# Optimization experiments

Measured on AMD Instinct MI355X. Metric: run time of the kernel, lower is better.

Reference implementation:

```python
import jax, jax.numpy as jnp
import numpy as np

NEG_SLOPE = 0.2  # PyG GATConv default LeakyReLU slope


def _leaky_relu(x):
    return jnp.where(x >= 0, x, NEG_SLOPE * x)


def gat_conv(x, edge_index, W, a_src, a_dst, b, concat):
    """Faithful PyG GATConv: gather -> leakyrelu attention -> per-dst softmax -> scatter.
    x: [N, Fin], edge_index: [2, E] (src, dst), W: [Fin, H*C], a_src/a_dst: [H, C], b: [H*C] or [C].
    """
    N = x.shape[0]
    H, C = a_src.shape
    src, dst = edge_index[0], edge_index[1]
    h = (x @ W).reshape(N, H, C)                       # [N, H, C]
    alpha_s = jnp.einsum('nhc,hc->nh', h, a_src)       # [N, H]
    alpha_d = jnp.einsum('nhc,hc->nh', h, a_dst)       # [N, H]
    e = _leaky_relu(alpha_s[src] + alpha_d[dst])       # [E, H]
    # numerically stable softmax over edges grouped by destination node
    m = jax.ops.segment_max(e, dst, num_segments=N)    # [N, H]
    e = jnp.exp(e - m[dst])                            # [E, H]
    denom = jax.ops.segment_sum(e, dst, num_segments=N)  # [N, H]
    alpha = e / denom[dst]                             # [E, H]
    msg = h[src] * alpha[:, :, None]                   # [E, H, C]
    out = jax.ops.segment_sum(msg, dst, num_segments=N)  # [N, H, C]
    out = out.reshape(N, H * C) if concat else out.mean(axis=1)
    return out + b


def setup_inputs() -> dict:
    key = jax.random.key(0)
    ks = jax.random.split(key, 12)
    N, E, Fin, Fout = 100000, 1600000, 256, 40
    H1, C1 = 8, 8
    x = jax.random.normal(ks[0], (N, Fin), dtype=jnp.float32)
    edge_index = jax.random.randint(ks[1], (2, E), 0, N, dtype=jnp.int64)
    g = lambda k, shape: jax.random.normal(k, shape, dtype=jnp.float32) * np.float32(np.sqrt(2.0 / (shape[0] + shape[-1])))
    return {
        'x': x,
        'edge_index': edge_index,
        'W1': g(ks[2], (Fin, H1 * C1)),
        'a1_src': g(ks[3], (H1, C1)),
        'a1_dst': g(ks[4], (H1, C1)),
        'b1': jnp.zeros((H1 * C1,), dtype=jnp.float32),
        'W2': g(ks[5], (H1 * C1, Fout)),
        'a2_src': g(ks[6], (1, Fout)),
        'a2_dst': g(ks[7], (1, Fout)),
        'b2': jnp.zeros((Fout,), dtype=jnp.float32),
    }


def reference(x, edge_index, W1, a1_src, a1_dst, b1, W2, a2_src, a2_dst, b2):
    N = x.shape[0]
    # PyG GATConv adds self-loops by default
    loops = jnp.arange(N, dtype=edge_index.dtype)
    ei = jnp.concatenate([edge_index, jnp.stack([loops, loops])], axis=1)
    h = gat_conv(x, ei, W1, a1_src, a1_dst, b1, concat=True)   # [N, 64]
    h = jax.nn.relu(h)  # F.dropout is identity in eval mode
    h = gat_conv(h, ei, W2, a2_src, a2_dst, b2, concat=False)  # [N, Fout]
    return jax.nn.log_softmax(h, axis=1)
```

## Files before the change

kernel.cpp:

```cpp
#include <hip/hip_runtime.h>
#include <math.h>

#define NEG_SLOPE 0.2f
__device__ __forceinline__ float lrelu(float x){ return x >= 0.f ? x : NEG_SLOPE * x; }

typedef __attribute__((ext_vector_type(8))) short bf16x8;
typedef __attribute__((ext_vector_type(4))) float f32x4;

__device__ __forceinline__ float wred_sum(float v){
  #pragma unroll
  for (int o = 32; o; o >>= 1) v += __shfl_xor(v, o, 64);
  return v;
}

__device__ __forceinline__ float bfhi_f(float f){
  return __uint_as_float(__float_as_uint(f) & 0xFFFF0000u);
}
__device__ __forceinline__ unsigned short f2bf(float f){
  unsigned u = __float_as_uint(f);
  unsigned r = u + 0x7FFFu + ((u >> 16) & 1u);
  return (unsigned short)(r >> 16);
}

__global__ __launch_bounds__(256) void k_bincnt(const int* __restrict__ ei, int E, int N, int nb,
                                                unsigned* __restrict__ bcnt){
  __shared__ unsigned h[512];
  const int tot = E + N;
  for (int i = threadIdx.x; i < nb; i += 256) h[i] = 0;
  __syncthreads();
  int base = blockIdx.x * 8192;
  #pragma unroll 4
  for (int j = 0; j < 32; j++){
    int e = base + threadIdx.x + j * 256;
    if (e < tot){
      unsigned d = (e < E) ? (unsigned)ei[E + e] : (unsigned)(e - E);
      atomicAdd(&h[d >> 8], 1u);
    }
  }
  __syncthreads();
  for (int i = threadIdx.x; i < nb; i += 256)
    if (h[i]) atomicAdd(&bcnt[i], h[i]);
}

__global__ void k_bscan(const unsigned* __restrict__ bcnt, unsigned* __restrict__ bbase,
                        unsigned* __restrict__ bcur, int nb, int tot){
  __shared__ unsigned s[512];
  int t = threadIdx.x;
  unsigned v = (t < nb) ? bcnt[t] : 0u;
  s[t] = v; __syncthreads();
  for (int off = 1; off < 512; off <<= 1){
    unsigned x = (t >= off) ? s[t - off] : 0u; __syncthreads();
    s[t] += x; __syncthreads();
  }
  if (t < nb){ unsigned b = s[t] - v; bbase[t] = b; bcur[t] = b; }
  if (t == 0) bbase[nb] = (unsigned)tot;
}

__global__ __launch_bounds__(256) void k_binscat(const int* __restrict__ ei, int E, int N, int nb,
    unsigned* __restrict__ bcur, unsigned* __restrict__ staged){
  __shared__ unsigned sd[8192];
  __shared__ unsigned hist[512];
  __shared__ unsigned runb[512];
  const int tot = E + N;
  for (int i = threadIdx.x; i < nb; i += 256) hist[i] = 0;
  __syncthreads();
  int base = blockIdx.x * 8192;
  #pragma unroll 4
  for (int j = 0; j < 32; j++){
    int idx = threadIdx.x + j * 256;
    int e = base + idx;
    unsigned d = 0xFFFFFFFFu;
    if (e < tot) d = (e < E) ? (unsigned)ei[E + e] : (unsigned)(e - E);
    sd[idx] = d;
    if (d != 0xFFFFFFFFu) atomicAdd(&hist[d >> 8], 1u);
  }
  __syncthreads();
  for (int i = threadIdx.x; i < nb; i += 256){
    unsigned c = hist[i];
    runb[i] = c ? atomicAdd(&bcur[i], c) : 0u;
    hist[i] = 0;
  }
  __syncthreads();
  #pragma unroll 4
  for (int j = 0; j < 32; j++){
    int idx = threadIdx.x + j * 256;
    unsigned d = sd[idx];
    if (d == 0xFFFFFFFFu) continue;
    int e = base + idx;
    unsigned s = (e < E) ? (unsigned)ei[e] : d;
    unsigned b = d >> 8;
    unsigned pos = runb[b] + atomicAdd(&hist[b], 1u);
    staged[pos] = s | ((d & 255u) << 20);
  }
}

__global__ __launch_bounds__(256) void k_csr(const unsigned* __restrict__ bbase,
    const unsigned* __restrict__ staged, int N,
    unsigned* __restrict__ off_, unsigned* __restrict__ cur, int* __restrict__ srcids){
  __shared__ unsigned cnt[256], scn[256], cnt2[256];
  int b = blockIdx.x, t = threadIdx.x;
  unsigned beg = bbase[b], end = bbase[b + 1];
  cnt[t] = 0; cnt2[t] = 0;
  __syncthreads();
  for (unsigned i = beg + t; i < end; i += 256)
    atomicAdd(&cnt[staged[i] >> 20], 1u);
  __syncthreads();
  unsigned v = cnt[t];
  scn[t] = v; __syncthreads();
  for (int off = 1; off < 256; off <<= 1){
    unsigned x = (t >= off) ? scn[t - off] : 0u; __syncthreads();
    scn[t] += x; __syncthreads();
  }
  unsigned ex = scn[t] - v;
  int d = b * 256 + t;
  if (d < N){ off_[d] = beg + ex; cur[d] = beg + ex + v; }
  cnt[t] = ex;
  __syncthreads();
  for (unsigned i = beg + t; i < end; i += 256){
    unsigned u = staged[i];
    unsigned dl = u >> 20;
    unsigned pos = beg + cnt[dl] + atomicAdd(&cnt2[dl], 1u);
    srcids[pos] = (int)(u & 0xFFFFFu);
  }
}

__global__ void k_wprep(const float* __restrict__ W, short* __restrict__ wt_hi,
                        short* __restrict__ wt_lo){
  int i = blockIdx.x * 256 + threadIdx.x;
  int k = i >> 6, c = i & 63;
  float v = W[i];
  unsigned u = __float_as_uint(v);
  wt_hi[c * 256 + k] = (short)(u >> 16);
  float lo = v - bfhi_f(v);
  wt_lo[c * 256 + k] = (short)(__float_as_uint(lo) >> 16);
}

__global__ void k_w2prep(const float* __restrict__ W2, short* __restrict__ hi,
                         short* __restrict__ lo){
  int i = blockIdx.x * 256 + threadIdx.x;
  if (i >= 48 * 64) return;
  int c = i >> 6, k = i & 63;
  float v = (c < 40) ? W2[k * 40 + c] : 0.f;
  unsigned u = __float_as_uint(v);
  hi[c * 64 + k] = (short)(u >> 16);
  float l = v - bfhi_f(v);
  lo[c * 64 + k] = (short)(__float_as_uint(l) >> 16);
}

__global__ __launch_bounds__(256) void k_gemm1_mfma(const float* __restrict__ x,
    const short* __restrict__ wt_hi, const short* __restrict__ wt_lo,
    const float* __restrict__ a1s, const float* __restrict__ a1d,
    unsigned short* __restrict__ h1b, float* __restrict__ as_, float* __restrict__ ad_, int N){
  int lane = threadIdx.x & 63;
  int wv   = threadIdx.x >> 6;
  int r0   = blockIdx.x * 64 + wv * 16;
  if (r0 >= N) return;
  int col16 = lane & 15;
  int kg    = lane >> 4;
  const float4* xr = (const float4*)(x + (size_t)min(r0 + col16, N - 1) * 256 + kg * 8);

  float4 xv[16];
  #pragma unroll
  for (int kt = 0; kt < 8; kt++){
    xv[2 * kt]     = xr[kt * 8];
    xv[2 * kt + 1] = xr[kt * 8 + 1];
  }

  f32x4 acc[4];
  #pragma unroll
  for (int ct = 0; ct < 4; ct++) acc[ct] = (f32x4){0.f, 0.f, 0.f, 0.f};

  #pragma unroll
  for (int kt = 0; kt < 8; kt++){
    float4 v0 = xv[2 * kt], v1 = xv[2 * kt + 1];
    unsigned u[8] = {__float_as_uint(v0.x), __float_as_uint(v0.y), __float_as_uint(v0.z), __float_as_uint(v0.w),
                     __float_as_uint(v1.x), __float_as_uint(v1.y), __float_as_uint(v1.z), __float_as_uint(v1.w)};
    union { bf16x8 v; unsigned u[4]; } ahi, alo;
    #pragma unroll
    for (int j = 0; j < 4; j++)
      ahi.u[j] = __builtin_amdgcn_perm(u[2*j+1], u[2*j], 0x07060302);
    float lo[8];
    lo[0] = v0.x - bfhi_f(v0.x); lo[1] = v0.y - bfhi_f(v0.y);
    lo[2] = v0.z - bfhi_f(v0.z); lo[3] = v0.w - bfhi_f(v0.w);
    lo[4] = v1.x - bfhi_f(v1.x); lo[5] = v1.y - bfhi_f(v1.y);
    lo[6] = v1.z - bfhi_f(v1.z); lo[7] = v1.w - bfhi_f(v1.w);
    #pragma unroll
    for (int j = 0; j < 4; j++)
      alo.u[j] = __builtin_amdgcn_perm(__float_as_uint(lo[2*j+1]), __float_as_uint(lo[2*j]), 0x07060302);

    #pragma unroll
    for (int ct = 0; ct < 4; ct++){
      int wcol = ct * 16 + col16;
      const bf16x8 bhi = *(const bf16x8*)(wt_hi + wcol * 256 + kt * 32 + kg * 8);
      const bf16x8 blo = *(const bf16x8*)(wt_lo + wcol * 256 + kt * 32 + kg * 8);
      acc[ct] = __builtin_amdgcn_mfma_f32_16x16x32_bf16(ahi.v, bhi, acc[ct], 0, 0, 0);
      acc[ct] = __builtin_amdgcn_mfma_f32_16x16x32_bf16(ahi.v, blo, acc[ct], 0, 0, 0);
      acc[ct] = __builtin_amdgcn_mfma_f32_16x16x32_bf16(alo.v, bhi, acc[ct], 0, 0, 0);
    }
  }

  float cs[4], cd[4];
  #pragma unroll
  for (int ct = 0; ct < 4; ct++){ cs[ct] = a1s[ct * 16 + col16]; cd[ct] = a1d[ct * 16 + col16]; }
  #pragma unroll
  for (int r = 0; r < 4; r++){
    int rr = r0 + kg * 4 + r;
    bool ok = rr < N;
    #pragma unroll
    for (int ct = 0; ct < 4; ct++){
      float v = acc[ct][r];
      if (ok) h1b[(size_t)rr * 64 + ct * 16 + col16] = f2bf(v);
      float s = v * cs[ct];
      float t = v * cd[ct];
      s += __shfl_xor(s, 1, 64); s += __shfl_xor(s, 2, 64); s += __shfl_xor(s, 4, 64);
      t += __shfl_xor(t, 1, 64); t += __shfl_xor(t, 2, 64); t += __shfl_xor(t, 4, 64);
      if (ok && (col16 & 7) == 0){
        int head = ct * 2 + (col16 >> 3);
        as_[(size_t)rr * 8 + head] = s;
        ad_[(size_t)rr * 8 + head] = t;
      }
    }
  }
}

__global__ __launch_bounds__(256) void k_gat1(const unsigned* __restrict__ off_, const unsigned* __restrict__ cur,
    const int* __restrict__ srcids, const float* __restrict__ as_, const float* __restrict__ ad_,
    const unsigned short* __restrict__ h1b, const float* __restrict__ b1,
    unsigned short* __restrict__ out1b, int N){
  int lane = threadIdx.x & 63;
  int wv   = threadIdx.x >> 6;
  int d    = blockIdx.x * 4 + wv;
  if (d >= N) return;
  __shared__ float lds_p[4][64 * 8];
  __shared__ int   lds_s[4][64];
  float* lp = lds_p[wv];
  int*   ls = lds_s[wv];
  unsigned beg = off_[d], fin = cur[d];

  int e8 = lane >> 3, h = lane & 7;
  int c0 = lane & 31, pe = lane >> 5, hh = c0 >> 2;
  float adh = ad_[(size_t)d * 8 + h];
  float psacc = 0.f, accx = 0.f, accy = 0.f;

  for (unsigned base = beg; base < fin; base += 64){
    int nthis = (int)min(64u, fin - base);
    unsigned i = base + lane;
    ls[lane] = (i < fin) ? srcids[i] : 0;
    asm volatile("s_waitcnt lgkmcnt(0)" ::: "memory");
    __builtin_amdgcn_sched_barrier(0);
    for (int j = 0; j < nthis; j += 8){
      int eloc = j + e8;
      int s = ls[eloc];
      float p = 0.f;
      if (eloc < nthis) p = __expf(lrelu(as_[(size_t)s * 8 + h] + adh));
      lp[eloc * 8 + h] = p;
      psacc += p;
    }
    asm volatile("s_waitcnt lgkmcnt(0)" ::: "memory");
    __builtin_amdgcn_sched_barrier(0);
    for (int e = 0; e < nthis; e += 8){
      int e0 = e + pe, e1 = e + 2 + pe, e2 = e + 4 + pe, e3 = e + 6 + pe;
      float p0 = lp[e0 * 8 + hh], p1 = lp[e1 * 8 + hh];
      float p2 = lp[e2 * 8 + hh], p3 = lp[e3 * 8 + hh];
      int s0 = ls[e0], s1 = ls[e1], s2 = ls[e2], s3 = ls[e3];
      unsigned u0 = *(const unsigned*)(h1b + (size_t)s0 * 64 + c0 * 2);
      unsigned u1 = *(const unsigned*)(h1b + (size_t)s1 * 64 + c0 * 2);
      unsigned u2 = *(const unsigned*)(h1b + (size_t)s2 * 64 + c0 * 2);
      unsigned u3 = *(const unsigned*)(h1b + (size_t)s3 * 64 + c0 * 2);
      accx = fmaf(p0, __uint_as_float(u0 << 16), accx);
      accy = fmaf(p0, __uint_as_float(u0 & 0xFFFF0000u), accy);
      accx = fmaf(p1, __uint_as_float(u1 << 16), accx);
      accy = fmaf(p1, __uint_as_float(u1 & 0xFFFF0000u), accy);
      accx = fmaf(p2, __uint_as_float(u2 << 16), accx);
      accy = fmaf(p2, __uint_as_float(u2 & 0xFFFF0000u), accy);
      accx = fmaf(p3, __uint_as_float(u3 << 16), accx);
      accy = fmaf(p3, __uint_as_float(u3 & 0xFFFF0000u), accy);
    }
    asm volatile("" ::: "memory");
  }
  float den = psacc;
  den += __shfl_xor(den, 8, 64);
  den += __shfl_xor(den, 16, 64);
  den += __shfl_xor(den, 32, 64);
  float mydenv = __shfl(den, hh, 64);
  accx += __shfl_xor(accx, 32, 64);
  accy += __shfl_xor(accy, 32, 64);
  if (lane < 32){
    int ch = lane * 2;
    float v0 = accx / mydenv + b1[ch];
    float v1 = accy / mydenv + b1[ch + 1];
    ushort2 o;
    o.x = f2bf(v0 > 0.f ? v0 : 0.f);
    o.y = f2bf(v1 > 0.f ? v1 : 0.f);
    *(ushort2*)(out1b + (size_t)d * 64 + ch) = o;
  }
}

__global__ __launch_bounds__(256) void k_gemm2m(const unsigned short* __restrict__ out1b,
    const short* __restrict__ wt2_hi, const short* __restrict__ wt2_lo,
    const float* __restrict__ a2s, const float* __restrict__ a2d,
    unsigned short* __restrict__ h2b, float* __restrict__ as_, float* __restrict__ ad_, int N){
  int lane = threadIdx.x & 63;
  int wv   = threadIdx.x >> 6;
  int r0   = blockIdx.x * 64 + wv * 16;
  if (r0 >= N) return;
  int col16 = lane & 15;
  int kg    = lane >> 4;
  const unsigned short* ar = out1b + (size_t)min(r0 + col16, N - 1) * 64 + kg * 8;

  f32x4 acc[3];
  #pragma unroll
  for (int ct = 0; ct < 3; ct++) acc[ct] = (f32x4){0.f, 0.f, 0.f, 0.f};

  #pragma unroll
  for (int kt = 0; kt < 2; kt++){
    const bf16x8 a = *(const bf16x8*)(ar + kt * 32);
    #pragma unroll
    for (int ct = 0; ct < 3; ct++){
      int wcol = ct * 16 + col16;
      const bf16x8 bhi = *(const bf16x8*)(wt2_hi + wcol * 64 + kt * 32 + kg * 8);
      const bf16x8 blo = *(const bf16x8*)(wt2_lo + wcol * 64 + kt * 32 + kg * 8);
      acc[ct] = __builtin_amdgcn_mfma_f32_16x16x32_bf16(a, bhi, acc[ct], 0, 0, 0);
      acc[ct] = __builtin_amdgcn_mfma_f32_16x16x32_bf16(a, blo, acc[ct], 0, 0, 0);
    }
  }

  float cs[3], cd[3];
  #pragma unroll
  for (int ct = 0; ct < 3; ct++){
    int col = ct * 16 + col16;
    bool okc = col < 40;
    cs[ct] = okc ? a2s[col] : 0.f;
    cd[ct] = okc ? a2d[col] : 0.f;
  }
  #pragma unroll
  for (int r = 0; r < 4; r++){
    int rr = r0 + kg * 4 + r;
    bool ok = rr < N;
    float s = 0.f, t = 0.f;
    #pragma unroll
    for (int ct = 0; ct < 3; ct++){
      s = fmaf(acc[ct][r], cs[ct], s);
      t = fmaf(acc[ct][r], cd[ct], t);
      int col = ct * 16 + col16;
      if (ok && col < 40) h2b[(size_t)rr * 40 + col] = f2bf(acc[ct][r]);
    }
    s += __shfl_xor(s, 1, 64); s += __shfl_xor(s, 2, 64);
    s += __shfl_xor(s, 4, 64); s += __shfl_xor(s, 8, 64);
    t += __shfl_xor(t, 1, 64); t += __shfl_xor(t, 2, 64);
    t += __shfl_xor(t, 4, 64); t += __shfl_xor(t, 8, 64);
    if (ok && col16 == 0){ as_[rr] = s; ad_[rr] = t; }
  }
}

__global__ __launch_bounds__(256) void k_gat2(const unsigned* __restrict__ off_, const unsigned* __restrict__ cur,
    const int* __restrict__ srcids, const float* __restrict__ as_, const float* __restrict__ ad_,
    const unsigned short* __restrict__ h2b, const float* __restrict__ b2, float* __restrict__ out, int N){
  int lane = threadIdx.x & 63;
  int wv   = threadIdx.x >> 6;
  int d    = blockIdx.x * 4 + wv;
  if (d >= N) return;
  __shared__ float lds_p[4][64];
  __shared__ int   lds_s[4][64];
  float* lp = lds_p[wv];
  int*   ls = lds_s[wv];
  unsigned beg = off_[d], fin = cur[d];
  float add = ad_[d];

  int c0 = lane & 31;
  int pe = lane >> 5;
  int idx = c0 < 20 ? c0 : 19;
  float ps = 0.f, accx = 0.f, accy = 0.f;

  for (unsigned base = beg; base < fin; base += 64){
    unsigned i = base + lane;
    int nthis = (int)min(64u, fin - base);
    if (i < fin){
      int s = srcids[i];
      float p = __expf(lrelu(as_[s] + add));
      ps += p; ls[lane] = s; lp[lane] = p;
    } else { ls[lane] = 0; lp[lane] = 0.f; }
    asm volatile("s_waitcnt lgkmcnt(0)" ::: "memory");
    __builtin_amdgcn_sched_barrier(0);
    for (int e = 0; e < nthis; e += 8){
      int e0 = e + pe, e1 = e + 2 + pe, e2 = e + 4 + pe, e3 = e + 6 + pe;
      float p0 = lp[e0], p1 = lp[e1], p2 = lp[e2], p3 = lp[e3];
      int s0 = ls[e0], s1 = ls[e1], s2 = ls[e2], s3 = ls[e3];
      unsigned u0 = *(const unsigned*)(h2b + (size_t)s0 * 40 + idx * 2);
      unsigned u1 = *(const unsigned*)(h2b + (size_t)s1 * 40 + idx * 2);
      unsigned u2 = *(const unsigned*)(h2b + (size_t)s2 * 40 + idx * 2);
      unsigned u3 = *(const unsigned*)(h2b + (size_t)s3 * 40 + idx * 2);
      accx = fmaf(p0, __uint_as_float(u0 << 16), accx);
      accy = fmaf(p0, __uint_as_float(u0 & 0xFFFF0000u), accy);
      accx = fmaf(p1, __uint_as_float(u1 << 16), accx);
      accy = fmaf(p1, __uint_as_float(u1 & 0xFFFF0000u), accy);
      accx = fmaf(p2, __uint_as_float(u2 << 16), accx);
      accy = fmaf(p2, __uint_as_float(u2 & 0xFFFF0000u), accy);
      accx = fmaf(p3, __uint_as_float(u3 << 16), accx);
      accy = fmaf(p3, __uint_as_float(u3 & 0xFFFF0000u), accy);
    }
    asm volatile("" ::: "memory");
  }
  ps = wred_sum(ps);
  accx += __shfl_xor(accx, 32, 64);
  accy += __shfl_xor(accy, 32, 64);

  float v0 = accx / ps + b2[idx * 2];
  float v1 = accy / ps + b2[idx * 2 + 1];
  bool act = (c0 < 20);
  float mx = act ? fmaxf(v0, v1) : -INFINITY;
  #pragma unroll
  for (int o = 16; o; o >>= 1) mx = fmaxf(mx, __shfl_xor(mx, o, 64));
  float exs = act ? (__expf(v0 - mx) + __expf(v1 - mx)) : 0.f;
  #pragma unroll
  for (int o = 16; o; o >>= 1) exs += __shfl_xor(exs, o, 64);
  float lse = mx + logf(exs);
  if (lane < 20){
    float2 o2; o2.x = v0 - lse; o2.y = v1 - lse;
    *(float2*)(out + (size_t)d * 40 + lane * 2) = o2;
  }
}

extern "C" void kernel_launch(void* const* d_in, const int* in_sizes, int n_in,
                              void* d_out, int out_size, void* d_ws, size_t ws_size,
                              hipStream_t stream){
  const float* x   = (const float*)d_in[0];
  const int*   ei  = (const int*)d_in[1];
  const float* W1  = (const float*)d_in[2];
  const float* a1s = (const float*)d_in[3];
  const float* a1d = (const float*)d_in[4];
  const float* b1  = (const float*)d_in[5];
  const float* W2  = (const float*)d_in[6];
  const float* a2s = (const float*)d_in[7];
  const float* a2d = (const float*)d_in[8];
  const float* b2  = (const float*)d_in[9];
  float* out = (float*)d_out;

  const int N = in_sizes[0] / 256;
  const int E = in_sizes[1] / 2;
  const int tot = E + N;
  const int nb  = (N + 255) >> 8;

  float* ws = (float*)d_ws;
  size_t o = 0;
  float* as1  = ws + o; o += (size_t)N * 8;
  float* ad1  = ws + o; o += (size_t)N * 8;
  unsigned short* out1b = (unsigned short*)(ws + o); o += (size_t)N * 32;
  unsigned short* h1b   = (unsigned short*)(ws + o); o += (size_t)N * 32;
  unsigned short* h2b   = (unsigned short*)(ws + o); o += (size_t)N * 20;
  unsigned* off_ = (unsigned*)(ws + o); o += (size_t)N;
  unsigned* cur  = (unsigned*)(ws + o); o += (size_t)N;
  int* srcids    = (int*)(ws + o);      o += (size_t)tot;
  short* wt_hi   = (short*)(ws + o);    o += 8192;
  short* wt_lo   = (short*)(ws + o);    o += 8192;
  short* wt2_hi  = (short*)(ws + o);    o += 1536;
  short* wt2_lo  = (short*)(ws + o);    o += 1536;
  unsigned* bcnt  = (unsigned*)(ws + o); o += nb;
  unsigned* bbase = (unsigned*)(ws + o); o += nb + 1;
  unsigned* bcur  = (unsigned*)(ws + o); o += nb;
  unsigned* staged = (unsigned*)out1b;
  float* as2 = as1;
  float* ad2 = ad1;

  const int cb = (tot + 8191) / 8192;

  hipMemsetAsync(bcnt, 0, sizeof(unsigned) * (size_t)nb, stream);

  k_bincnt <<<cb, 256, 0, stream>>>(ei, E, N, nb, bcnt);
  k_bscan  <<<1, 512, 0, stream>>>(bcnt, bbase, bcur, nb, tot);
  k_binscat<<<cb, 256, 0, stream>>>(ei, E, N, nb, bcur, staged);
  k_csr    <<<nb, 256, 0, stream>>>(bbase, staged, N, off_, cur, srcids);

  k_wprep <<<64, 256, 0, stream>>>(W1, wt_hi, wt_lo);
  k_w2prep<<<12, 256, 0, stream>>>(W2, wt2_hi, wt2_lo);

  k_gemm1_mfma<<<(N + 63) / 64, 256, 0, stream>>>(x, wt_hi, wt_lo, a1s, a1d, h1b, as1, ad1, N);
  k_gat1 <<<(N + 3) / 4, 256, 0, stream>>>(off_, cur, srcids, as1, ad1, h1b, b1, out1b, N);

  k_gemm2m<<<(N + 63) / 64, 256, 0, stream>>>(out1b, wt2_hi, wt2_lo, a2s, a2d, h2b, as2, ad2, N);
  k_gat2  <<<(N + 3) / 4, 256, 0, stream>>>(off_, cur, srcids, as2, ad2, h2b, b2, out, N);
}
```

Baseline: 266.5 us.

## Stream x tiles into LDS with async global_load_lds double buffering

The first-layer GEMM now copies x rows straight into per-wave LDS buffers with global_load_lds, in four 64-column chunks with double buffering, instead of loading all 16 float4 into registers up front. Each chunk is read back from swizzled LDS to build the bf16 hi/lo MFMA operands while the next chunk is in flight. This aims to overlap global loads with MFMA work, coalesce the x reads and cut register pressure, at the cost of 32KB of LDS per block and manual vmcnt waits that could reduce occupancy.

```diff
diff --git a/kernel.cpp b/kernel.cpp
--- a/kernel.cpp
+++ b/kernel.cpp
@@ -151,52 +151,82 @@
     const short* __restrict__ wt_hi, const short* __restrict__ wt_lo,
     const float* __restrict__ a1s, const float* __restrict__ a1d,
     unsigned short* __restrict__ h1b, float* __restrict__ as_, float* __restrict__ ad_, int N){
+  __shared__ float lds[4][2][1024];
   int lane = threadIdx.x & 63;
   int wv   = threadIdx.x >> 6;
   int r0   = blockIdx.x * 64 + wv * 16;
   if (r0 >= N) return;
   int col16 = lane & 15;
   int kg    = lane >> 4;
-  const float4* xr = (const float4*)(x + (size_t)min(r0 + col16, N - 1) * 256 + kg * 8);
-
-  float4 xv[16];
-  #pragma unroll
-  for (int kt = 0; kt < 8; kt++){
-    xv[2 * kt]     = xr[kt * 8];
-    xv[2 * kt + 1] = xr[kt * 8 + 1];
-  }
+  int srl   = lane >> 4;
+  int sci   = lane & 15;
 
   f32x4 acc[4];
   #pragma unroll
   for (int ct = 0; ct < 4; ct++) acc[ct] = (f32x4){0.f, 0.f, 0.f, 0.f};
 
   #pragma unroll
-  for (int kt = 0; kt < 8; kt++){
-    float4 v0 = xv[2 * kt], v1 = xv[2 * kt + 1];
-    unsigned u[8] = {__float_as_uint(v0.x), __float_as_uint(v0.y), __float_as_uint(v0.z), __float_as_uint(v0.w),
-                     __float_as_uint(v1.x), __float_as_uint(v1.y), __float_as_uint(v1.z), __float_as_uint(v1.w)};
-    union { bf16x8 v; unsigned u[4]; } ahi, alo;
+  for (int ri = 0; ri < 4; ri++){
+    int rl = ri * 4 + srl;
+    int ci = sci ^ (rl & 7);
+    const float* gsrc = x + (size_t)min(r0 + rl, N - 1) * 256 + ci * 4;
+    float* ldst = &lds[wv][0][ri * 256];
+    __builtin_amdgcn_global_load_lds((const __attribute__((address_space(1))) void*)(const void*)gsrc,
+                                     (__attribute__((address_space(3))) void*)(void*)ldst, 16, 0, 0);
+  }
+
+  int buf = 0;
+  for (int ch = 0; ch < 4; ch++){
+    if (ch < 3){
+      #pragma unroll
+      for (int ri = 0; ri < 4; ri++){
+        int rl = ri * 4 + srl;
+        int ci = sci ^ (rl & 7);
+        const float* gsrc = x + (size_t)min(r0 + rl, N - 1) * 256 + (ch + 1) * 64 + ci * 4;
+        float* ldst = &lds[wv][buf ^ 1][ri * 256];
+        __builtin_amdgcn_global_load_lds((const __attribute__((address_space(1))) void*)(const void*)gsrc,
+                                         (__attribute__((address_space(3))) void*)(void*)ldst, 16, 0, 0);
+      }
+      asm volatile("s_waitcnt vmcnt(4)" ::: "memory");
+    } else {
+      asm volatile("s_waitcnt vmcnt(0)" ::: "memory");
+    }
+    __builtin_amdgcn_sched_barrier(0);
+
+    const float* wb = &lds[wv][buf][0];
     #pragma unroll
-    for (int j = 0; j < 4; j++)
-      ahi.u[j] = __builtin_amdgcn_perm(u[2*j+1], u[2*j], 0x07060302);
-    float lo[8];
-    lo[0] = v0.x - bfhi_f(v0.x); lo[1] = v0.y - bfhi_f(v0.y);
-    lo[2] = v0.z - bfhi_f(v0.z); lo[3] = v0.w - bfhi_f(v0.w);
-    lo[4] = v1.x - bfhi_f(v1.x); lo[5] = v1.y - bfhi_f(v1.y);
-    lo[6] = v1.z - bfhi_f(v1.z); lo[7] = v1.w - bfhi_f(v1.w);
-    #pragma unroll
-    for (int j = 0; j < 4; j++)
-      alo.u[j] = __builtin_amdgcn_perm(__float_as_uint(lo[2*j+1]), __float_as_uint(lo[2*j]), 0x07060302);
-
-    #pragma unroll
-    for (int ct = 0; ct < 4; ct++){
-      int wcol = ct * 16 + col16;
-      const bf16x8 bhi = *(const bf16x8*)(wt_hi + wcol * 256 + kt * 32 + kg * 8);
-      const bf16x8 blo = *(const bf16x8*)(wt_lo + wcol * 256 + kt * 32 + kg * 8);
-      acc[ct] = __builtin_amdgcn_mfma_f32_16x16x32_bf16(ahi.v, bhi, acc[ct], 0, 0, 0);
-      acc[ct] = __builtin_amdgcn_mfma_f32_16x16x32_bf16(ahi.v, blo, acc[ct], 0, 0, 0);
-      acc[ct] = __builtin_amdgcn_mfma_f32_16x16x32_bf16(alo.v, bhi, acc[ct], 0, 0, 0);
-    }
+    for (int kt = 0; kt < 2; kt++){
+      int b16 = kt * 8 + kg * 2;
+      int swz = col16 & 7;
+      float4 v0 = *(const float4*)(wb + col16 * 64 + (((b16 + 0) ^ swz) << 2));
+      float4 v1 = *(const float4*)(wb + col16 * 64 + (((b16 + 1) ^ swz) << 2));
+      unsigned u[8] = {__float_as_uint(v0.x), __float_as_uint(v0.y), __float_as_uint(v0.z), __float_as_uint(v0.w),
+                       __float_as_uint(v1.x), __float_as_uint(v1.y), __float_as_uint(v1.z), __float_as_uint(v1.w)};
+      union { bf16x8 v; unsigned u[4]; } ahi, alo;
+      #pragma unroll
+      for (int j = 0; j < 4; j++)
+        ahi.u[j] = __builtin_amdgcn_perm(u[2*j+1], u[2*j], 0x07060302);
+      float lo[8];
+      lo[0] = v0.x - bfhi_f(v0.x); lo[1] = v0.y - bfhi_f(v0.y);
+      lo[2] = v0.z - bfhi_f(v0.z); lo[3] = v0.w - bfhi_f(v0.w);
+      lo[4] = v1.x - bfhi_f(v1.x); lo[5] = v1.y - bfhi_f(v1.y);
+      lo[6] = v1.z - bfhi_f(v1.z); lo[7] = v1.w - bfhi_f(v1.w);
+      #pragma unroll
+      for (int j = 0; j < 4; j++)
+        alo.u[j] = __builtin_amdgcn_perm(__float_as_uint(lo[2*j+1]), __float_as_uint(lo[2*j]), 0x07060302);
+
+      int ktg = ch * 2 + kt;
+      #pragma unroll
+      for (int ct = 0; ct < 4; ct++){
+        int wcol = ct * 16 + col16;
+        const bf16x8 bhi = *(const bf16x8*)(wt_hi + wcol * 256 + ktg * 32 + kg * 8);
+        const bf16x8 blo = *(const bf16x8*)(wt_lo + wcol * 256 + ktg * 32 + kg * 8);
+        acc[ct] = __builtin_amdgcn_mfma_f32_16x16x32_bf16(ahi.v, bhi, acc[ct], 0, 0, 0);
+        acc[ct] = __builtin_amdgcn_mfma_f32_16x16x32_bf16(ahi.v, blo, acc[ct], 0, 0, 0);
+        acc[ct] = __builtin_amdgcn_mfma_f32_16x16x32_bf16(alo.v, bhi, acc[ct], 0, 0, 0);
+      }
+    }
+    buf ^= 1;
   }
 
   float cs[4], cd[4];
```

Result: no change. 261.8 us (-1.7%).
